# Performance work log

Measured on AMD Instinct MI355X. Metric: run time of the kernel, lower is better.

## Reference

```python
import jax, jax.numpy as jnp
import numpy as np

EPS = 1e-6
H, A, V = 4, 64, 64  # heads, attn_dim, hidden_dim


def layer_norm(x, w, b):
    mu = jnp.mean(x, axis=-1, keepdims=True)
    var = jnp.var(x, axis=-1, keepdims=True)
    return (x - mu) * jax.lax.rsqrt(var + EPS) * w + b


def setup_inputs() -> dict:
    key = jax.random.key(0)
    B, N, D = 4, 2048, 512
    lengths = np.array([2048, 1536, 1024, 1792], np.int32)
    offsets = np.concatenate([[0], np.cumsum(lengths)]).astype(np.int32)
    L = int(offsets[-1])  # 6400
    uvqk_out = (2 * V + 2 * A) * H  # 1024
    out_in = 2 * V * H + D          # concat([u, x, normed_attn])
    ks = jax.random.split(key, 4)
    return {
        "x": jax.random.normal(ks[0], (L, D), jnp.float32),
        "x_lengths": jnp.asarray(lengths),
        "x_offsets": jnp.asarray(offsets),
        "max_seq_len": N,
        "num_targets": jnp.asarray([32, 16, 8, 64], jnp.int32),
        "uvqk_weight": jax.random.normal(ks[1], (D, uvqk_out), jnp.float32) / np.float32(np.sqrt(D)),
        "uvqk_bias": jnp.zeros((uvqk_out,), jnp.float32),
        "input_norm_weight": jnp.ones((D,), jnp.float32),
        "input_norm_bias": jnp.zeros((D,), jnp.float32),
        "output_norm_weight": jnp.ones((V * H,), jnp.float32),
        "output_norm_bias": jnp.zeros((V * H,), jnp.float32),
        "output_weight": jax.random.normal(ks[2], (out_in, D), jnp.float32) / np.float32(np.sqrt(out_in)),
    }


def reference(x, x_lengths, x_offsets, max_seq_len, num_targets,
              uvqk_weight, uvqk_bias, input_norm_weight, input_norm_bias,
              output_norm_weight, output_norm_bias, output_weight):
    L, D = x.shape
    B = x_lengths.shape[0]
    N = int(max_seq_len)
    alpha = A ** -0.5

    # fused input layernorm + UVQK projection + silu
    nx = layer_norm(x, input_norm_weight, input_norm_bias)
    uvqk = jax.nn.silu(nx @ uvqk_weight + uvqk_bias)              # [L, (2V+2A)*H]
    u = uvqk[:, : V * H]                                          # [L, V*H]
    v = uvqk[:, V * H: 2 * V * H].reshape(L, H, V)
    q = uvqk[:, 2 * V * H: 2 * V * H + A * H].reshape(L, H, A)
    k = uvqk[:, 2 * V * H + A * H:].reshape(L, H, A)

    # jagged -> padded [B, N, ...]
    pos = jnp.arange(N)
    gather_idx = jnp.clip(x_offsets[:-1, None] + pos[None, :], 0, L - 1)  # [B,N]
    valid = pos[None, :] < x_lengths[:, None]                              # [B,N]
    qp = q[gather_idx] * valid[..., None, None]
    kp = k[gather_idx] * valid[..., None, None]
    vp = v[gather_idx] * valid[..., None, None]

    # target-aware causal mask: clamp ids at uih boundary; eye | dist>0
    max_ids = (x_lengths - num_targets)[:, None]        # [B,1]
    ids = jnp.minimum(pos[None, :], max_ids)            # [B,N]
    dist = ids[:, :, None] - ids[:, None, :]            # [B,N,N]
    mask = (dist > 0) | jnp.eye(N, dtype=bool)[None]
    mask = mask & valid[:, :, None] & valid[:, None, :]

    scores = jnp.einsum("bnha,bmha->bhnm", qp, kp) * alpha
    attn_w = jax.nn.silu(scores) * (1.0 / N)
    attn_w = attn_w * mask[:, None].astype(attn_w.dtype)
    attn_p = jnp.einsum("bhnm,bmhv->bnhv", attn_w, vp).reshape(B, N, H * V)

    # padded -> jagged
    tok = jnp.arange(L)
    b_of = jnp.searchsorted(x_offsets, tok, side="right") - 1
    p_of = tok - x_offsets[b_of]
    attn = attn_p[b_of, p_of]                            # [L, H*V]

    # output: norm(attn), concat [u, x, y], project, residual (dropout off / eval)
    y = layer_norm(attn, output_norm_weight, output_norm_bias)
    y = jnp.concatenate([u, x, y], axis=1)
    return x + y @ output_weight
```

## Files before the change

### kernel.cpp

```cpp
#include <hip/hip_runtime.h>
#include <math.h>

#define NSEQ 2048
#define PIT 72

typedef __attribute__((ext_vector_type(8))) short short8;
typedef __attribute__((ext_vector_type(4))) short short4v;
typedef __attribute__((ext_vector_type(4))) float f32x4;

__device__ __forceinline__ float silu_f(float z) {
    return z * __builtin_amdgcn_rcpf(1.f + __expf(-z));
}

__device__ __forceinline__ unsigned short f2bf(float f) {
    unsigned int u = __float_as_uint(f);
    u += 0x7fffu + ((u >> 16) & 1u);
    return (unsigned short)(u >> 16);
}

__device__ __forceinline__ unsigned short f2bf_fast(float f) {
    return (unsigned short)((__float_as_uint(f) + 0x8000u) >> 16);
}

__device__ __forceinline__ short8 scale8_pow2(short8 v, float s) {
    short8 r;
    #pragma unroll
    for (int i = 0; i < 8; i++) {
        float f = __uint_as_float(((unsigned int)(unsigned short)v[i]) << 16) * s;
        r[i] = (short)(unsigned short)(__float_as_uint(f) >> 16);
    }
    return r;
}

__global__ void __launch_bounds__(256) transpose_to_bf16(
    const float* __restrict__ W, unsigned short* __restrict__ Wt, int R, int C)
{
    __shared__ float t[32][33];
    int tid = threadIdx.x;
    int tr = tid >> 5, tc = tid & 31;
    int r0 = blockIdx.y * 32, c0 = blockIdx.x * 32;
    #pragma unroll
    for (int p = 0; p < 4; p++)
        t[tr + p * 8][tc] = W[(size_t)(r0 + tr + p * 8) * C + c0 + tc];
    __syncthreads();
    #pragma unroll
    for (int p = 0; p < 4; p++)
        Wt[(size_t)(c0 + tr + p * 8) * R + r0 + tc] = f2bf(t[tc][tr + p * 8]);
}

__global__ void __launch_bounds__(256) ln512_kernel(
    const float* __restrict__ x, const float* __restrict__ w,
    const float* __restrict__ b,
    unsigned short* __restrict__ nxb, unsigned short* __restrict__ A2)
{
    int tid = threadIdx.x;
    int r = tid >> 7;
    int row = blockIdx.x * 2 + r;
    int c = (tid & 127) * 4;
    float4 v = *(const float4*)(x + (size_t)row * 512 + c);
    float s = v.x + v.y + v.z + v.w;
    float sq = v.x * v.x + v.y * v.y + v.z * v.z + v.w * v.w;
    for (int o = 32; o > 0; o >>= 1) { s += __shfl_down(s, o); sq += __shfl_down(sq, o); }
    __shared__ float red[8];
    int wv = tid >> 6;
    if ((tid & 63) == 0) { red[wv] = s; red[4 + wv] = sq; }
    __syncthreads();
    float ts = red[2 * r] + red[2 * r + 1];
    float tq = red[4 + 2 * r] + red[4 + 2 * r + 1];
    float mu = ts * (1.f / 512.f);
    float var = tq * (1.f / 512.f) - mu * mu;
    float rs = rsqrtf(var + 1e-6f);
    float4 wv4 = *(const float4*)(w + c);
    float4 bv4 = *(const float4*)(b + c);
    ushort4 hn, hx;
    hn.x = f2bf((v.x - mu) * rs * wv4.x + bv4.x);
    hn.y = f2bf((v.y - mu) * rs * wv4.y + bv4.y);
    hn.z = f2bf((v.z - mu) * rs * wv4.z + bv4.z);
    hn.w = f2bf((v.w - mu) * rs * wv4.w + bv4.w);
    hx.x = f2bf(v.x); hx.y = f2bf(v.y); hx.z = f2bf(v.z); hx.w = f2bf(v.w);
    *(ushort4*)(nxb + (size_t)row * 512 + c) = hn;
    *(ushort4*)(A2 + (size_t)row * 1024 + 256 + c) = hx;
}

__global__ void __launch_bounds__(256) ln256_kernel(
    const float* __restrict__ a, const float* __restrict__ w,
    const float* __restrict__ b, unsigned short* __restrict__ A2)
{
    int tid = threadIdx.x;
    int r = tid >> 7;
    int row = blockIdx.x * 2 + r;
    int c = (tid & 127) * 2;
    float2 v = *(const float2*)(a + (size_t)row * 256 + c);
    float s = v.x + v.y, sq = v.x * v.x + v.y * v.y;
    for (int o = 32; o > 0; o >>= 1) { s += __shfl_down(s, o); sq += __shfl_down(sq, o); }
    __shared__ float red[8];
    int wv = tid >> 6;
    if ((tid & 63) == 0) { red[wv] = s; red[4 + wv] = sq; }
    __syncthreads();
    float ts = red[2 * r] + red[2 * r + 1];
    float tq = red[4 + 2 * r] + red[4 + 2 * r + 1];
    float mu = ts * (1.f / 256.f);
    float var = tq * (1.f / 256.f) - mu * mu;
    float rs = rsqrtf(var + 1e-6f);
    float2 w2 = *(const float2*)(w + c);
    float2 b2 = *(const float2*)(b + c);
    ushort2 h;
    h.x = f2bf((v.x - mu) * rs * w2.x + b2.x);
    h.y = f2bf((v.y - mu) * rs * w2.y + b2.y);
    *(ushort2*)(A2 + (size_t)row * 1024 + 768 + c) = h;
}

__global__ void __launch_bounds__(256) gemm1_mfma(
    const unsigned short* __restrict__ Ab, const unsigned short* __restrict__ Bt,
    const float* __restrict__ bias,
    unsigned short* __restrict__ A2, unsigned short* __restrict__ qkvb)
{
    constexpr int K = 512, KIT = K / 64;
    __shared__ unsigned short As[64 * PIT];
    __shared__ unsigned short Bs[128 * PIT];
    int tid = threadIdx.x, lane = tid & 63, w = tid >> 6;
    int wr = w >> 1, wc = w & 1;
    int nn = lane & 15, qd = lane >> 4;
    int bm = blockIdx.y * 64, bn = blockIdx.x * 128;
    int arow = tid >> 2, ac0 = (tid & 3) * 16;
    int brow = tid >> 1, bc0 = (tid & 1) * 32;
    const unsigned short* Ag = Ab + (size_t)(bm + arow) * K + ac0;
    const unsigned short* Bg = Bt + (size_t)(bn + brow) * K + bc0;

    short8 pa0 = *(const short8*)Ag, pa1 = *(const short8*)(Ag + 8);
    short8 pb0 = *(const short8*)Bg, pb1 = *(const short8*)(Bg + 8);
    short8 pb2 = *(const short8*)(Bg + 16), pb3 = *(const short8*)(Bg + 24);

    f32x4 acc[2][4];
    #pragma unroll
    for (int i = 0; i < 2; i++)
        #pragma unroll
        for (int j = 0; j < 4; j++) acc[i][j] = (f32x4){0.f, 0.f, 0.f, 0.f};

    for (int it = 0; it < KIT; ++it) {
        __syncthreads();
        *(short8*)&As[arow * PIT + ac0]     = pa0;
        *(short8*)&As[arow * PIT + ac0 + 8] = pa1;
        *(short8*)&Bs[brow * PIT + bc0]      = pb0;
        *(short8*)&Bs[brow * PIT + bc0 + 8]  = pb1;
        *(short8*)&Bs[brow * PIT + bc0 + 16] = pb2;
        *(short8*)&Bs[brow * PIT + bc0 + 24] = pb3;
        __syncthreads();
        if (it + 1 < KIT) {
            int k0 = (it + 1) * 64;
            pa0 = *(const short8*)(Ag + k0); pa1 = *(const short8*)(Ag + k0 + 8);
            pb0 = *(const short8*)(Bg + k0); pb1 = *(const short8*)(Bg + k0 + 8);
            pb2 = *(const short8*)(Bg + k0 + 16); pb3 = *(const short8*)(Bg + k0 + 24);
        }
        #pragma unroll
        for (int kk = 0; kk < 2; kk++) {
            short8 af[2], bf[4];
            #pragma unroll
            for (int i = 0; i < 2; i++)
                af[i] = *(const short8*)&As[(wr * 32 + i * 16 + nn) * PIT + kk * 32 + qd * 8];
            #pragma unroll
            for (int j = 0; j < 4; j++)
                bf[j] = *(const short8*)&Bs[(wc * 64 + j * 16 + nn) * PIT + kk * 32 + qd * 8];
            #pragma unroll
            for (int i = 0; i < 2; i++)
                #pragma unroll
                for (int j = 0; j < 4; j++)
                    acc[i][j] = __builtin_amdgcn_mfma_f32_16x16x32_bf16(af[i], bf[j], acc[i][j], 0, 0, 0);
        }
    }
    bool isU = (bn < 256);
    #pragma unroll
    for (int j = 0; j < 4; j++) {
        int col = bn + wc * 64 + j * 16 + nn;
        float bb = bias[col];
        #pragma unroll
        for (int i = 0; i < 2; i++) {
            int rbase = bm + wr * 32 + i * 16 + qd * 4;
            #pragma unroll
            for (int r = 0; r < 4; r++) {
                unsigned short hh = f2bf(silu_f(acc[i][j][r] + bb));
                if (isU) A2[(size_t)(rbase + r) * 1024 + col] = hh;
                else     qkvb[(size_t)(rbase + r) * 768 + col - 256] = hh;
            }
        }
    }
}

__global__ void __launch_bounds__(256) gemm2_mfma(
    const unsigned short* __restrict__ Ab, const unsigned short* __restrict__ Bt,
    const float* __restrict__ x, float* __restrict__ out)
{
    constexpr int K = 1024, KIT = K / 64;
    __shared__ unsigned short As[64 * PIT];
    __shared__ unsigned short Bs[128 * PIT];
    int tid = threadIdx.x, lane = tid & 63, w = tid >> 6;
    int wr = w >> 1, wc = w & 1;
    int nn = lane & 15, qd = lane >> 4;
    int bm = blockIdx.y * 64, bn = blockIdx.x * 128;
    int arow = tid >> 2, ac0 = (tid & 3) * 16;
    int brow = tid >> 1, bc0 = (tid & 1) * 32;
    const unsigned short* Ag = Ab + (size_t)(bm + arow) * K + ac0;
    const unsigned short* Bg = Bt + (size_t)(bn + brow) * K + bc0;

    short8 pa0 = *(const short8*)Ag, pa1 = *(const short8*)(Ag + 8);
    short8 pb0 = *(const short8*)Bg, pb1 = *(const short8*)(Bg + 8);
    short8 pb2 = *(const short8*)(Bg + 16), pb3 = *(const short8*)(Bg + 24);

    f32x4 acc[2][4];
    #pragma unroll
    for (int i = 0; i < 2; i++)
        #pragma unroll
        for (int j = 0; j < 4; j++) acc[i][j] = (f32x4){0.f, 0.f, 0.f, 0.f};

    for (int it = 0; it < KIT; ++it) {
        __syncthreads();
        *(short8*)&As[arow * PIT + ac0]     = pa0;
        *(short8*)&As[arow * PIT + ac0 + 8] = pa1;
        *(short8*)&Bs[brow * PIT + bc0]      = pb0;
        *(short8*)&Bs[brow * PIT + bc0 + 8]  = pb1;
        *(short8*)&Bs[brow * PIT + bc0 + 16] = pb2;
        *(short8*)&Bs[brow * PIT + bc0 + 24] = pb3;
        __syncthreads();
        if (it + 1 < KIT) {
            int k0 = (it + 1) * 64;
            pa0 = *(const short8*)(Ag + k0); pa1 = *(const short8*)(Ag + k0 + 8);
            pb0 = *(const short8*)(Bg + k0); pb1 = *(const short8*)(Bg + k0 + 8);
            pb2 = *(const short8*)(Bg + k0 + 16); pb3 = *(const short8*)(Bg + k0 + 24);
        }
        #pragma unroll
        for (int kk = 0; kk < 2; kk++) {
            short8 af[2], bf[4];
            #pragma unroll
            for (int i = 0; i < 2; i++)
                af[i] = *(const short8*)&As[(wr * 32 + i * 16 + nn) * PIT + kk * 32 + qd * 8];
            #pragma unroll
            for (int j = 0; j < 4; j++)
                bf[j] = *(const short8*)&Bs[(wc * 64 + j * 16 + nn) * PIT + kk * 32 + qd * 8];
            #pragma unroll
            for (int i = 0; i < 2; i++)
                #pragma unroll
                for (int j = 0; j < 4; j++)
                    acc[i][j] = __builtin_amdgcn_mfma_f32_16x16x32_bf16(af[i], bf[j], acc[i][j], 0, 0, 0);
        }
    }
    #pragma unroll
    for (int j = 0; j < 4; j++) {
        int col = bn + wc * 64 + j * 16 + nn;
        #pragma unroll
        for (int i = 0; i < 2; i++) {
            int rbase = bm + wr * 32 + i * 16 + qd * 4;
            #pragma unroll
            for (int r = 0; r < 4; r++) {
                size_t idx = (size_t)(rbase + r) * 512 + col;
                out[idx] = x[idx] + acc[i][j][r];
            }
        }
    }
}

__global__ void __launch_bounds__(256, 2) attn_mfma_kernel(
    const unsigned short* __restrict__ qkvb,
    const int* __restrict__ offsets,
    const int* __restrict__ lengths,
    const int* __restrict__ num_targets,
    float* __restrict__ attn)
{
    int bh = blockIdx.y;
    int b = bh >> 2, h = bh & 3;
    int len = lengths[b];
    int n0 = (31 - (int)blockIdx.x) * 64;
    if (n0 >= len) return;
    int m_hi = min(n0 + 63, len - 1);
    int off = offsets[b];
    int max_id = len - num_targets[b];
    int tid = threadIdx.x, lane = tid & 63, w = tid >> 6;
    int nn = lane & 15, qd = lane >> 4;

    __shared__ __align__(16) char smem[69632];
    unsigned short* Vt = (unsigned short*)(smem + w * 9216);
    float* Os = (float*)smem;

    short8 qf[4][2];
    #pragma unroll
    for (int g = 0; g < 4; g++) {
        int row = min(n0 + g * 16 + nn, len - 1);
        const unsigned short* base = qkvb + (size_t)(off + row) * 768 + 256 + h * 64;
        qf[g][0] = scale8_pow2(*(const short8*)(base + qd * 8), 0.125f);
        qf[g][1] = scale8_pow2(*(const short8*)(base + 32 + qd * 8), 0.125f);
    }

    f32x4 o_acc[4][4];
    #pragma unroll
    for (int t = 0; t < 4; t++)
        #pragma unroll
        for (int g = 0; g < 4; g++) o_acc[t][g] = (f32x4){0.f, 0.f, 0.f, 0.f};

    int fast_lim = min(n0, max_id);
    int r0 = (lane & 15) * 4, d0 = (lane >> 4) * 16;

    short8 kf[4][2], kn[4][2], vf[4][2];
    int m_first = w * 64;
    if (m_first <= m_hi) {
        #pragma unroll
        for (int s = 0; s < 4; s++) {
            int row = min(m_first + s * 16 + nn, len - 1);
            const unsigned short* kb = qkvb + (size_t)(off + row) * 768 + 512 + h * 64 + qd * 8;
            kf[s][0] = *(const short8*)kb;
            kf[s][1] = *(const short8*)(kb + 32);
        }
        #pragma unroll
        for (int j = 0; j < 4; j++) {
            int row = min(m_first + r0 + j, len - 1);
            const unsigned short* vb = qkvb + (size_t)(off + row) * 768 + h * 64 + d0;
            vf[j][0] = *(const short8*)vb;
            vf[j][1] = *(const short8*)(vb + 8);
        }
    }

    for (int m0 = m_first; m0 <= m_hi; m0 += 256) {
        #pragma unroll
        for (int dd = 0; dd < 16; dd++) {
            int hh = dd >> 3, e = dd & 7;
            short4v pk;
            pk[0] = vf[0][hh][e]; pk[1] = vf[1][hh][e];
            pk[2] = vf[2][hh][e]; pk[3] = vf[3][hh][e];
            *(short4v*)&Vt[(d0 + dd) * PIT + r0] = pk;
        }
        int mnext = m0 + 256;
        if (mnext <= m_hi) {
            #pragma unroll
            for (int j = 0; j < 4; j++) {
                int row = min(mnext + r0 + j, len - 1);
                const unsigned short* vb = qkvb + (size_t)(off + row) * 768 + h * 64 + d0;
                vf[j][0] = *(const short8*)vb;
                vf[j][1] = *(const short8*)(vb + 8);
            }
            #pragma unroll
            for (int s = 0; s < 4; s++) {
                int row = min(mnext + s * 16 + nn, len - 1);
                const unsigned short* kb = qkvb + (size_t)(off + row) * 768 + 512 + h * 64 + qd * 8;
                kn[s][0] = *(const short8*)kb;
                kn[s][1] = *(const short8*)(kb + 32);
            }
        }
        bool fastp = (m0 + 63 < fast_lim);
        #pragma unroll
        for (int s = 0; s < 4; s++) {
            f32x4 st[4];
            #pragma unroll
            for (int g = 0; g < 4; g++) {
                st[g] = (f32x4){0.f, 0.f, 0.f, 0.f};
                st[g] = __builtin_amdgcn_mfma_f32_16x16x32_bf16(kf[s][0], qf[g][0], st[g], 0, 0, 0);
                st[g] = __builtin_amdgcn_mfma_f32_16x16x32_bf16(kf[s][1], qf[g][1], st[g], 0, 0, 0);
            }
            short4v bop[4];
            if (fastp) {
                #pragma unroll
                for (int g = 0; g < 4; g++)
                    #pragma unroll
                    for (int r = 0; r < 4; r++)
                        bop[g][r] = (short)f2bf_fast(silu_f(st[g][r]));
            } else {
                #pragma unroll
                for (int g = 0; g < 4; g++) {
                    int nc_ = n0 + g * 16 + nn;
                    int id_ = min(nc_, max_id);
                    #pragma unroll
                    for (int r = 0; r < 4; r++) {
                        int mcol = m0 + s * 16 + qd * 4 + r;
                        bool ok = (mcol < id_) || (mcol == nc_);
                        bop[g][r] = (short)f2bf_fast(ok ? silu_f(st[g][r]) : 0.f);
                    }
                }
            }
            #pragma unroll
            for (int t = 0; t < 4; t++) {
                short4v aop = *(const short4v*)&Vt[(t * 16 + nn) * PIT + s * 16 + qd * 4];
                #pragma unroll
                for (int g = 0; g < 4; g++)
                    o_acc[t][g] = __builtin_amdgcn_mfma_f32_16x16x16bf16_1k(aop, bop[g], o_acc[t][g], 0, 0, 0);
            }
        }
        if (mnext <= m_hi) {
            #pragma unroll
            for (int s = 0; s < 4; s++) { kf[s][0] = kn[s][0]; kf[s][1] = kn[s][1]; }
        }
    }

    __syncthreads();
    const float invN = 1.f / (float)NSEQ;
    float* Ow = Os + w * 4352;
    #pragma unroll
    for (int t = 0; t < 4; t++)
        #pragma unroll
        for (int g = 0; g < 4; g++) {
            f32x4 v = o_acc[t][g] * invN;
            *(f32x4*)&Ow[(g * 16 + nn) * 68 + t * 16 + qd * 4] = v;
        }
    __syncthreads();
    int rr = tid >> 2, cs = (tid & 3) * 16;
    if (n0 + rr < len) {
        float* dst = attn + (size_t)(off + n0 + rr) * 256 + h * 64 + cs;
        #pragma unroll
        for (int q4 = 0; q4 < 4; q4++) {
            f32x4 v = (f32x4){0.f, 0.f, 0.f, 0.f};
            #pragma unroll
            for (int w2 = 0; w2 < 4; w2++)
                v += *(const f32x4*)&Os[w2 * 4352 + rr * 68 + cs + q4 * 4];
            *(f32x4*)(dst + q4 * 4) = v;
        }
    }
}

extern "C" void kernel_launch(void* const* d_in, const int* in_sizes, int n_in,
                              void* d_out, int out_size, void* d_ws, size_t ws_size,
                              hipStream_t stream)
{
    const float* x          = (const float*)d_in[0];
    const int*   x_lengths  = (const int*)d_in[1];
    const int*   x_offsets  = (const int*)d_in[2];
    const int*   num_targets = (const int*)d_in[4];
    const float* uvqk_w     = (const float*)d_in[5];
    const float* uvqk_b     = (const float*)d_in[6];
    const float* in_w       = (const float*)d_in[7];
    const float* in_b       = (const float*)d_in[8];
    const float* out_w      = (const float*)d_in[9];
    const float* out_b      = (const float*)d_in[10];
    const float* Wo         = (const float*)d_in[11];
    float* out = (float*)d_out;

    int L = in_sizes[0] / 512;
    int B = in_sizes[1];

    char* ws = (char*)d_ws;
    size_t o = 0;
    float* attn = (float*)(ws + o);          o += (size_t)L * 256 * 4;
    unsigned short* nxb  = (unsigned short*)(ws + o); o += (size_t)L * 512 * 2;
    unsigned short* A2   = (unsigned short*)(ws + o); o += (size_t)L * 1024 * 2;
    unsigned short* qkvb = (unsigned short*)(ws + o); o += (size_t)L * 768 * 2;
    unsigned short* W1t  = (unsigned short*)(ws + o); o += (size_t)1024 * 512 * 2;
    unsigned short* W2t  = (unsigned short*)(ws + o); o += (size_t)512 * 1024 * 2;

    transpose_to_bf16<<<dim3(1024 / 32, 512 / 32), 256, 0, stream>>>(uvqk_w, W1t, 512, 1024);
    transpose_to_bf16<<<dim3(512 / 32, 1024 / 32), 256, 0, stream>>>(Wo, W2t, 1024, 512);

    ln512_kernel<<<L / 2, 256, 0, stream>>>(x, in_w, in_b, nxb, A2);

    dim3 g1(1024 / 128, L / 64);
    gemm1_mfma<<<g1, 256, 0, stream>>>(nxb, W1t, uvqk_b, A2, qkvb);

    dim3 g2(NSEQ / 64, 16);
    attn_mfma_kernel<<<g2, 256, 0, stream>>>(qkvb, x_offsets, x_lengths, num_targets, attn);

    ln256_kernel<<<L / 2, 256, 0, stream>>>(attn, out_w, out_b, A2);

    dim3 g3(512 / 128, L / 64);
    gemm2_mfma<<<g3, 256, 0, stream>>>(A2, W2t, x, out);
}
```

Before: 170.0 us.

## Merge weight transposes, use wave-per-row layernorms, reorder attention grid, add MFMA priority

The two weight-transpose launches are merged into one kernel that picks its matrix from the block index, which removes a launch. Both layernorm kernels now give each wavefront a whole row, so the reduction is a pure xor-shuffle with no shared memory or barrier. The attention grid is flattened to 1D with batch-head as the fastest index, so the longest query tiles of all sequences are scheduled first. s_setprio hints are placed around the MFMA sections to favour matrix issue over the silu and mask code.

```diff
diff --git a/kernel.cpp b/kernel.cpp
--- a/kernel.cpp
+++ b/kernel.cpp
@@ -32,13 +32,18 @@
     return r;
 }
 
-__global__ void __launch_bounds__(256) transpose_to_bf16(
-    const float* __restrict__ W, unsigned short* __restrict__ Wt, int R, int C)
+__global__ void __launch_bounds__(256) transpose_both(
+    const float* __restrict__ W1, unsigned short* __restrict__ W1t,
+    const float* __restrict__ W2, unsigned short* __restrict__ W2t)
 {
     __shared__ float t[32][33];
+    int id = blockIdx.x;
+    const float* W; unsigned short* Wt; int R, C, bx, by;
+    if (id < 512) { W = W1; Wt = W1t; R = 512;  C = 1024; bx = id & 31; by = id >> 5; }
+    else { id -= 512; W = W2; Wt = W2t; R = 1024; C = 512;  bx = id & 15; by = id >> 4; }
     int tid = threadIdx.x;
     int tr = tid >> 5, tc = tid & 31;
-    int r0 = blockIdx.y * 32, c0 = blockIdx.x * 32;
+    int r0 = by * 32, c0 = bx * 32;
     #pragma unroll
     for (int p = 0; p < 4; p++)
         t[tr + p * 8][tc] = W[(size_t)(r0 + tr + p * 8) * C + c0 + tc];
@@ -53,61 +58,62 @@
     const float* __restrict__ b,
     unsigned short* __restrict__ nxb, unsigned short* __restrict__ A2)
 {
-    int tid = threadIdx.x;
-    int r = tid >> 7;
-    int row = blockIdx.x * 2 + r;
-    int c = (tid & 127) * 4;
-    float4 v = *(const float4*)(x + (size_t)row * 512 + c);
-    float s = v.x + v.y + v.z + v.w;
-    float sq = v.x * v.x + v.y * v.y + v.z * v.z + v.w * v.w;
-    for (int o = 32; o > 0; o >>= 1) { s += __shfl_down(s, o); sq += __shfl_down(sq, o); }
-    __shared__ float red[8];
-    int wv = tid >> 6;
-    if ((tid & 63) == 0) { red[wv] = s; red[4 + wv] = sq; }
-    __syncthreads();
-    float ts = red[2 * r] + red[2 * r + 1];
-    float tq = red[4 + 2 * r] + red[4 + 2 * r + 1];
-    float mu = ts * (1.f / 512.f);
-    float var = tq * (1.f / 512.f) - mu * mu;
+    int tid = threadIdx.x, lane = tid & 63, wv = tid >> 6;
+    int row = blockIdx.x * 4 + wv;
+    int c = lane * 8;
+    const float* xr = x + (size_t)row * 512 + c;
+    float4 v0 = *(const float4*)xr;
+    float4 v1 = *(const float4*)(xr + 4);
+    float s  = v0.x + v0.y + v0.z + v0.w + v1.x + v1.y + v1.z + v1.w;
+    float sq = v0.x * v0.x + v0.y * v0.y + v0.z * v0.z + v0.w * v0.w
+             + v1.x * v1.x + v1.y * v1.y + v1.z * v1.z + v1.w * v1.w;
+    #pragma unroll
+    for (int o = 32; o > 0; o >>= 1) { s += __shfl_xor(s, o); sq += __shfl_xor(sq, o); }
+    float mu = s * (1.f / 512.f);
+    float var = sq * (1.f / 512.f) - mu * mu;
     float rs = rsqrtf(var + 1e-6f);
-    float4 wv4 = *(const float4*)(w + c);
-    float4 bv4 = *(const float4*)(b + c);
-    ushort4 hn, hx;
-    hn.x = f2bf((v.x - mu) * rs * wv4.x + bv4.x);
-    hn.y = f2bf((v.y - mu) * rs * wv4.y + bv4.y);
-    hn.z = f2bf((v.z - mu) * rs * wv4.z + bv4.z);
-    hn.w = f2bf((v.w - mu) * rs * wv4.w + bv4.w);
-    hx.x = f2bf(v.x); hx.y = f2bf(v.y); hx.z = f2bf(v.z); hx.w = f2bf(v.w);
-    *(ushort4*)(nxb + (size_t)row * 512 + c) = hn;
-    *(ushort4*)(A2 + (size_t)row * 1024 + 256 + c) = hx;
+    float4 w0 = *(const float4*)(w + c), w1 = *(const float4*)(w + c + 4);
+    float4 b0 = *(const float4*)(b + c), b1 = *(const float4*)(b + c + 4);
+    ushort4 hn0, hn1, hx0, hx1;
+    hn0.x = f2bf((v0.x - mu) * rs * w0.x + b0.x);
+    hn0.y = f2bf((v0.y - mu) * rs * w0.y + b0.y);
+    hn0.z = f2bf((v0.z - mu) * rs * w0.z + b0.z);
+    hn0.w = f2bf((v0.w - mu) * rs * w0.w + b0.w);
+    hn1.x = f2bf((v1.x - mu) * rs * w1.x + b1.x);
+    hn1.y = f2bf((v1.y - mu) * rs * w1.y + b1.y);
+    hn1.z = f2bf((v1.z - mu) * rs * w1.z + b1.z);
+    hn1.w = f2bf((v1.w - mu) * rs * w1.w + b1.w);
+    hx0.x = f2bf(v0.x); hx0.y = f2bf(v0.y); hx0.z = f2bf(v0.z); hx0.w = f2bf(v0.w);
+    hx1.x = f2bf(v1.x); hx1.y = f2bf(v1.y); hx1.z = f2bf(v1.z); hx1.w = f2bf(v1.w);
+    unsigned short* nr = nxb + (size_t)row * 512 + c;
+    *(ushort4*)nr = hn0; *(ushort4*)(nr + 4) = hn1;
+    unsigned short* ar = A2 + (size_t)row * 1024 + 256 + c;
+    *(ushort4*)ar = hx0; *(ushort4*)(ar + 4) = hx1;
 }
 
 __global__ void __launch_bounds__(256) ln256_kernel(
     const float* __restrict__ a, const float* __restrict__ w,
     const float* __restrict__ b, unsigned short* __restrict__ A2)
 {
-    int tid = threadIdx.x;
-    int r = tid >> 7;
-    int row = blockIdx.x * 2 + r;
-    int c = (tid & 127) * 2;
-    float2 v = *(const float2*)(a + (size_t)row * 256 + c);
-    float s = v.x + v.y, sq = v.x * v.x + v.y * v.y;
-    for (int o = 32; o > 0; o >>= 1) { s += __shfl_down(s, o); sq += __shfl_down(sq, o); }
-    __shared__ float red[8];
-    int wv = tid >> 6;
-    if ((tid & 63) == 0) { red[wv] = s; red[4 + wv] = sq; }
-    __syncthreads();
-    float ts = red[2 * r] + red[2 * r + 1];
-    float tq = red[4 + 2 * r] + red[4 + 2 * r + 1];
-    float mu = ts * (1.f / 256.f);
-    float var = tq * (1.f / 256.f) - mu * mu;
+    int tid = threadIdx.x, lane = tid & 63, wv = tid >> 6;
+    int row = blockIdx.x * 4 + wv;
+    int c = lane * 4;
+    float4 v = *(const float4*)(a + (size_t)row * 256 + c);
+    float s  = v.x + v.y + v.z + v.w;
+    float sq = v.x * v.x + v.y * v.y + v.z * v.z + v.w * v.w;
+    #pragma unroll
+    for (int o = 32; o > 0; o >>= 1) { s += __shfl_xor(s, o); sq += __shfl_xor(sq, o); }
+    float mu = s * (1.f / 256.f);
+    float var = sq * (1.f / 256.f) - mu * mu;
     float rs = rsqrtf(var + 1e-6f);
-    float2 w2 = *(const float2*)(w + c);
-    float2 b2 = *(const float2*)(b + c);
-    ushort2 h;
-    h.x = f2bf((v.x - mu) * rs * w2.x + b2.x);
-    h.y = f2bf((v.y - mu) * rs * w2.y + b2.y);
-    *(ushort2*)(A2 + (size_t)row * 1024 + 768 + c) = h;
+    float4 w4 = *(const float4*)(w + c);
+    float4 b4 = *(const float4*)(b + c);
+    ushort4 h;
+    h.x = f2bf((v.x - mu) * rs * w4.x + b4.x);
+    h.y = f2bf((v.y - mu) * rs * w4.y + b4.y);
+    h.z = f2bf((v.z - mu) * rs * w4.z + b4.z);
+    h.w = f2bf((v.w - mu) * rs * w4.w + b4.w);
+    *(ushort4*)(A2 + (size_t)row * 1024 + 768 + c) = h;
 }
 
 __global__ void __launch_bounds__(256) gemm1_mfma(
@@ -265,10 +271,12 @@
     const int* __restrict__ num_targets,
     float* __restrict__ attn)
 {
-    int bh = blockIdx.y;
+    int id = blockIdx.x;
+    int bh = id & 15;
+    int xt = id >> 4;
     int b = bh >> 2, h = bh & 3;
     int len = lengths[b];
-    int n0 = (31 - (int)blockIdx.x) * 64;
+    int n0 = (31 - xt) * 64;
     if (n0 >= len) return;
     int m_hi = min(n0 + 63, len - 1);
     int off = offsets[b];
@@ -347,12 +355,14 @@
         #pragma unroll
         for (int s = 0; s < 4; s++) {
             f32x4 st[4];
+            __builtin_amdgcn_s_setprio(1);
             #pragma unroll
             for (int g = 0; g < 4; g++) {
                 st[g] = (f32x4){0.f, 0.f, 0.f, 0.f};
                 st[g] = __builtin_amdgcn_mfma_f32_16x16x32_bf16(kf[s][0], qf[g][0], st[g], 0, 0, 0);
                 st[g] = __builtin_amdgcn_mfma_f32_16x16x32_bf16(kf[s][1], qf[g][1], st[g], 0, 0, 0);
             }
+            __builtin_amdgcn_s_setprio(0);
             short4v bop[4];
             if (fastp) {
                 #pragma unroll
@@ -373,6 +383,7 @@
                     }
                 }
             }
+            __builtin_amdgcn_s_setprio(1);
             #pragma unroll
             for (int t = 0; t < 4; t++) {
                 short4v aop = *(const short4v*)&Vt[(t * 16 + nn) * PIT + s * 16 + qd * 4];
@@ -380,6 +391,7 @@
                 for (int g = 0; g < 4; g++)
                     o_acc[t][g] = __builtin_amdgcn_mfma_f32_16x16x16bf16_1k(aop, bop[g], o_acc[t][g], 0, 0, 0);
             }
+            __builtin_amdgcn_s_setprio(0);
         }
         if (mnext <= m_hi) {
             #pragma unroll
@@ -441,18 +453,16 @@
     unsigned short* W1t  = (unsigned short*)(ws + o); o += (size_t)1024 * 512 * 2;
     unsigned short* W2t  = (unsigned short*)(ws + o); o += (size_t)512 * 1024 * 2;
 
-    transpose_to_bf16<<<dim3(1024 / 32, 512 / 32), 256, 0, stream>>>(uvqk_w, W1t, 512, 1024);
-    transpose_to_bf16<<<dim3(512 / 32, 1024 / 32), 256, 0, stream>>>(Wo, W2t, 1024, 512);
-
-    ln512_kernel<<<L / 2, 256, 0, stream>>>(x, in_w, in_b, nxb, A2);
+    transpose_both<<<dim3(1024), 256, 0, stream>>>(uvqk_w, W1t, Wo, W2t);
+
+    ln512_kernel<<<L / 4, 256, 0, stream>>>(x, in_w, in_b, nxb, A2);
 
     dim3 g1(1024 / 128, L / 64);
     gemm1_mfma<<<g1, 256, 0, stream>>>(nxb, W1t, uvqk_b, A2, qkvb);
 
-    dim3 g2(NSEQ / 64, 16);
-    attn_mfma_kernel<<<g2, 256, 0, stream>>>(qkvb, x_offsets, x_lengths, num_targets, attn);
-
-    ln256_kernel<<<L / 2, 256, 0, stream>>>(attn, out_w, out_b, A2);
+    attn_mfma_kernel<<<dim3(512), 256, 0, stream>>>(qkvb, x_offsets, x_lengths, num_targets, attn);
+
+    ln256_kernel<<<L / 4, 256, 0, stream>>>(attn, out_w, out_b, A2);
 
     dim3 g3(512 / 128, L / 64);
     gemm2_mfma<<<g3, 256, 0, stream>>>(A2, W2t, x, out);
```

Result: faster. 165.0 us (-2.9%).
